# Optimization experiments

Measured on AMD Instinct MI355X. Metric: run time of the kernel, lower is better.

The kernel has to match this reference:

```python
import jax, jax.numpy as jnp
import numpy as np
import math

B, S, E = 4, 2048, 1024
H, KV = 16, 4            # query heads, kv heads
HD = E // H              # head_dim = 64
R, CD = 8, 64            # TPA rank, context dim
NQ, NL = 8, 2            # qubits, VQC layers
EPS = 1e-6
LN_EPS = 1e-5


def setup_inputs() -> dict:
    key = jax.random.key(0)
    ks = jax.random.split(key, 16)
    def dense(k, i, o):
        return (jax.random.normal(k, (i, o), jnp.float32) / np.float32(np.sqrt(i)))
    d = {}
    d["x"] = jax.random.normal(ks[0], (B, S, E), jnp.float32)
    d["ctxW"] = dense(ks[1], E, CD);      d["ctxb"] = jnp.zeros((CD,), jnp.float32)
    d["qaW"] = dense(ks[2], E, R * HD);   d["qab"] = jnp.zeros((R * HD,), jnp.float32)
    d["qbW"] = dense(ks[3], CD, R * H);   d["qbb"] = jnp.zeros((R * H,), jnp.float32)
    d["kaW"] = dense(ks[4], E, R * HD);   d["kab"] = jnp.zeros((R * HD,), jnp.float32)
    d["kbW"] = dense(ks[5], CD, R * KV);  d["kbb"] = jnp.zeros((R * KV,), jnp.float32)
    d["vaW"] = dense(ks[6], E, R * HD);   d["vab"] = jnp.zeros((R * HD,), jnp.float32)
    d["vbW"] = dense(ks[7], CD, R * KV);  d["vbb"] = jnp.zeros((R * KV,), jnp.float32)
    d["qeW"] = dense(ks[8], HD, NQ);      d["qeb"] = jnp.zeros((NQ,), jnp.float32)
    d["vqc"] = jax.random.normal(ks[9], (NL, NQ, 3), jnp.float32) * 0.3
    d["ent"] = jnp.array([0.1], jnp.float32)
    d["outW"] = dense(ks[10], E, E);      d["outb"] = jnp.zeros((E,), jnp.float32)
    d["gamma"] = jnp.ones((E,), jnp.float32)
    d["beta"] = jnp.zeros((E,), jnp.float32)
    return d


def _tpa(x, ctx, aW, ab, bW, bb, nh):
    # output = sum_r (x @ A_r) outer (ctx @ B_r)  ->  [b, nh, s, head_dim]
    b, s, _ = x.shape
    a = (x @ aW + ab).reshape(b, s, R, HD)
    bf = (ctx @ bW + bb).reshape(b, s, R, nh)
    return jnp.einsum('bsrd,bsrh->bhsd', a, bf)


def _quantum_features(x, qeW, qeb, vqc, ent):
    # x: [b, h, s, HD] -> features [b, h, s, 2*NQ]
    angles = jnp.tanh(x @ qeW + qeb) * math.pi
    f = angles
    for l in range(NL):
        p = vqc[l]  # [NQ, 3]
        f = jnp.cos(f + p[:, 0]) * jnp.sin(f + p[:, 1]) + jnp.cos(f + p[:, 2])
        f = f * (1.0 + ent[0] * jnp.roll(f, shift=1, axis=-1))  # entanglement
    qf = jnp.concatenate([jnp.cos(f), jnp.sin(f)], axis=-1)
    return qf / (jnp.linalg.norm(qf, axis=-1, keepdims=True) + EPS)


def reference(x, ctxW, ctxb, qaW, qab, qbW, qbb, kaW, kab, kbW, kbb,
              vaW, vab, vbW, vbb, qeW, qeb, vqc, ent, outW, outb, gamma, beta):
    ctx = x @ ctxW + ctxb                              # [B,S,CD]
    q = _tpa(x, ctx, qaW, qab, qbW, qbb, H)            # [B,H,S,HD]
    k = _tpa(x, ctx, kaW, kab, kbW, kbb, KV)           # [B,KV,S,HD]
    v = _tpa(x, ctx, vaW, vab, vbW, vbb, KV)
    # GQA: expand KV heads to match query heads
    k = jnp.repeat(k, H // KV, axis=1)
    v = jnp.repeat(v, H // KV, axis=1)
    qf = _quantum_features(q, qeW, qeb, vqc, ent)      # [B,H,S,2*NQ]
    kf = _quantum_features(k, qeW, qeb, vqc, ent)
    # causal linear attention via cumulative KV state
    kv = jnp.cumsum(jnp.einsum('bhsf,bhsd->bhsfd', kf, v), axis=2)
    num = jnp.einsum('bhsf,bhsfd->bhsd', qf, kv)
    den = jnp.einsum('bhsf,bhsf->bhs', qf, jnp.cumsum(kf, axis=2))
    attn = num / (den[..., None] + EPS)                # [B,H,S,HD]
    o = attn.transpose(0, 2, 1, 3).reshape(B, S, E) @ outW + outb
    y = x + o                                          # residual + layernorm
    mu = jnp.mean(y, axis=-1, keepdims=True)
    var = jnp.mean(jnp.square(y - mu), axis=-1, keepdims=True)
    return gamma * (y - mu) / jnp.sqrt(var + LN_EPS) + beta
```

## Files before the change

kernel.cpp:

```cpp
#include <hip/hip_runtime.h>
#include <math.h>

#define Bb  4
#define Ss  2048
#define Ee  1024
#define Hh  16
#define KVh 4
#define HD  64
#define RNK 8
#define CDd 64
#define NQ  8
#define NLn 2
#define NF  16
#define NC  32
#define CT  (Ss/NC)
#define BS  (Bb*Ss)
#define NCAT 1664

typedef unsigned short ushort_t;
typedef __attribute__((ext_vector_type(8))) short short8;
typedef __attribute__((ext_vector_type(4))) float f32x4;

__device__ __forceinline__ unsigned short f2bf(float f) {
    unsigned int u = __float_as_uint(f);
    unsigned int r = (u + 0x7FFFu + ((u >> 16) & 1u)) >> 16;
    return (unsigned short)r;
}
__device__ __forceinline__ float bf2f(unsigned short h) {
    return __uint_as_float(((unsigned int)h) << 16);
}

#define GLD16(gp, lp) \
    __builtin_amdgcn_global_load_lds((const __attribute__((address_space(1))) void*)(gp), \
                                     (__attribute__((address_space(3))) void*)(lp), 16, 0, 0)

__global__ __launch_bounds__(256)
void cast_f32_bf16(const float* __restrict__ in, ushort_t* __restrict__ outp, long n)
{
    long i = ((long)blockIdx.x * blockDim.x + threadIdx.x) * 8;
    if (i >= n) return;
    short8 o;
    #pragma unroll
    for (int j = 0; j < 8; ++j) o[j] = (short)f2bf(in[i + j]);
    *(short8*)(outp + i) = o;
}

__global__ __launch_bounds__(256)
void transpose_cast(const float* __restrict__ W, ushort_t* __restrict__ Wt,
                    int K, int Nsub, int nOff, int ldT)
{
    __shared__ float t[32][33];
    const int k0 = blockIdx.x * 32, n0 = blockIdx.y * 32;
    const int tx = threadIdx.x & 31, ty = threadIdx.x >> 5;
    #pragma unroll
    for (int i = 0; i < 4; ++i)
        t[ty + 8*i][tx] = W[(size_t)(k0 + ty + 8*i) * Nsub + (n0 + tx)];
    __syncthreads();
    #pragma unroll
    for (int i = 0; i < 4; ++i)
        Wt[(size_t)(nOff + n0 + ty + 8*i) * ldT + (k0 + tx)] = f2bf(t[tx][ty + 8*i]);
}

__global__ __launch_bounds__(256)
void transpose_cast3(const float* __restrict__ W0, const float* __restrict__ W1,
                     const float* __restrict__ W2, ushort_t* __restrict__ Wt, int ldT)
{
    __shared__ float t[32][33];
    const int z = blockIdx.z;
    const float* W = (z == 0) ? W0 : (z == 1) ? W1 : W2;
    const int nOff = 512 * z;
    const int k0 = blockIdx.x * 32, n0 = blockIdx.y * 32;
    const int tx = threadIdx.x & 31, ty = threadIdx.x >> 5;
    #pragma unroll
    for (int i = 0; i < 4; ++i)
        t[ty + 8*i][tx] = W[(size_t)(k0 + ty + 8*i) * 512 + (n0 + tx)];
    __syncthreads();
    #pragma unroll
    for (int i = 0; i < 4; ++i)
        Wt[(size_t)(nOff + n0 + ty + 8*i) * ldT + (k0 + tx)] = f2bf(t[tx][ty + 8*i]);
}

__global__ void build_bcat(const float* __restrict__ qab, const float* __restrict__ kab,
                           const float* __restrict__ vab, const float* __restrict__ ctxb,
                           float* __restrict__ bcat)
{
    int n = blockIdx.x * 256 + threadIdx.x;
    if (n >= NCAT) return;
    float v = 0.f;
    if      (n < 512)  v = qab[n];
    else if (n < 1024) v = kab[n - 512];
    else if (n < 1536) v = vab[n - 1024];
    else if (n < 1600) v = ctxb[n - 1536];
    bcat[n] = v;
}

template<int RES, int OUTBF>
__global__ __launch_bounds__(256)
void gemm_mfma(const ushort_t* __restrict__ A, const ushort_t* __restrict__ Bt,
               const float* __restrict__ bias, const float* __restrict__ res,
               void* __restrict__ Cout, int M, int N, int K)
{
    __shared__ ushort_t Al[128 * 32];
    __shared__ ushort_t Bl[128 * 32];
    const int tid  = threadIdx.x;
    const int lane = tid & 63;
    const int wave = tid >> 6;
    const int wm = wave >> 1;
    const int wn = wave & 1;

    const unsigned nx  = gridDim.x;
    const unsigned bid = blockIdx.y * nx + blockIdx.x;
    const unsigned nwg = nx * gridDim.y;
    const unsigned qc = nwg >> 3, rc = nwg & 7;
    const unsigned xc = bid & 7, of = bid >> 3;
    const unsigned tile = (xc < rc ? xc * (qc + 1) : rc * (qc + 1) + (xc - rc) * qc) + of;
    const int bm = (int)(tile / nx) * 128;
    const int bn = (int)(tile % nx) * 128;

    f32x4 acc[4][4] = {};

    const int arow0 = wave * 16 + (lane >> 2);
    const int kq = lane & 3;
    const ushort_t* Ag0 = A  + (size_t)(bm + arow0) * K + kq * 8;
    const ushort_t* Ag1 = A  + (size_t)(bm + 64 + arow0) * K + kq * 8;
    const ushort_t* Bg0 = Bt + (size_t)(bn + arow0) * K + kq * 8;
    const ushort_t* Bg1 = Bt + (size_t)(bn + 64 + arow0) * K + kq * 8;
    ushort_t* Alw = Al + wave * 512;
    ushort_t* Blw = Bl + wave * 512;

    const int fr = lane & 15;
    const int fg = lane >> 4;

    for (int k0 = 0; k0 < K; k0 += 32) {
        GLD16(Ag0 + k0, Alw);
        GLD16(Ag1 + k0, Alw + 2048);
        GLD16(Bg0 + k0, Blw);
        GLD16(Bg1 + k0, Blw + 2048);
        __syncthreads();
        short8 af[4], bfv[4];
        #pragma unroll
        for (int mi = 0; mi < 4; ++mi)
            af[mi] = *(const short8*)&Al[(wm*64 + mi*16 + fr) * 32 + fg * 8];
        #pragma unroll
        for (int ni = 0; ni < 4; ++ni)
            bfv[ni] = *(const short8*)&Bl[(wn*64 + ni*16 + fr) * 32 + fg * 8];
        #pragma unroll
        for (int mi = 0; mi < 4; ++mi)
            #pragma unroll
            for (int ni = 0; ni < 4; ++ni)
                acc[mi][ni] = __builtin_amdgcn_mfma_f32_16x16x32_bf16(
                    af[mi], bfv[ni], acc[mi][ni], 0, 0, 0);
        __syncthreads();
    }

    float bv[4];
    #pragma unroll
    for (int ni = 0; ni < 4; ++ni) bv[ni] = bias[bn + wn*64 + ni*16 + fr];
    #pragma unroll
    for (int mi = 0; mi < 4; ++mi) {
        #pragma unroll
        for (int ni = 0; ni < 4; ++ni) {
            const int gn = bn + wn*64 + ni*16 + fr;
            #pragma unroll
            for (int r = 0; r < 4; ++r) {
                const int gm = bm + wm*64 + mi*16 + fg*4 + r;
                float v = acc[mi][ni][r] + bv[ni];
                if (RES) v += res[(size_t)gm * N + gn];
                if (OUTBF) ((ushort_t*)Cout)[(size_t)gm * N + gn] = f2bf(v);
                else       ((float*)Cout)[(size_t)gm * N + gn] = v;
            }
        }
    }
}

__global__ __launch_bounds__(64)
void combine_quantum(const ushort_t* __restrict__ Cf,
                     const float* __restrict__ qbW, const float* __restrict__ qbb,
                     const float* __restrict__ kbW, const float* __restrict__ kbb,
                     const float* __restrict__ vbW, const float* __restrict__ vbb,
                     const float* __restrict__ qeW, const float* __restrict__ qeb,
                     const float* __restrict__ vqc, const float* __restrict__ ent,
                     float* __restrict__ qf_g, float* __restrict__ kf_g,
                     float* __restrict__ v_g)
{
    const int bs = blockIdx.x;
    const int b = bs >> 11;
    const int s = bs & 2047;
    const int d = threadIdx.x;

    __shared__ float ctx_l[CDd];
    __shared__ float bfq[128];
    __shared__ float bfk[32];
    __shared__ float bfv[32];
    __shared__ float qew_s[HD*NQ];
    __shared__ float rows[Hh+KVh][65];
    __shared__ float ang[Hh+KVh][NQ];

    const ushort_t* Crow = Cf + (size_t)bs * NCAT;
    ctx_l[d] = bf2f(Crow[1536 + d]);
    #pragma unroll
    for (int i = 0; i < 8; ++i)
        qew_s[d + 64*i] = qeW[d + 64*i];
    __syncthreads();

    {
        float q0 = qbb[d], q1 = qbb[d + 64];
        float kv = (d < 32) ? kbb[d] : vbb[d - 32];
        const float* Wkv = (d < 32) ? (kbW + d) : (vbW + (d - 32));
        #pragma unroll 8
        for (int k = 0; k < CDd; ++k) {
            const float c = ctx_l[k];
            q0 += c * qbW[(size_t)k*128 + d];
            q1 += c * qbW[(size_t)k*128 + d + 64];
            kv += c * Wkv[(size_t)k*32];
        }
        bfq[d] = q0; bfq[d + 64] = q1;
        if (d < 32) bfk[d] = kv; else bfv[d - 32] = kv;
    }

    float aq[RNK], ak[RNK], av[RNK];
    #pragma unroll
    for (int r = 0; r < RNK; ++r) {
        aq[r] = bf2f(Crow[r*64 + d]);
        ak[r] = bf2f(Crow[512 + r*64 + d]);
        av[r] = bf2f(Crow[1024 + r*64 + d]);
    }
    __syncthreads();

    #pragma unroll
    for (int h = 0; h < Hh; ++h) {
        float acc = 0.f;
        #pragma unroll
        for (int r = 0; r < RNK; ++r) acc += aq[r] * bfq[r*16 + h];
        rows[h][d] = acc;
    }
    #pragma unroll
    for (int kvh = 0; kvh < KVh; ++kvh) {
        float acck = 0.f, accv = 0.f;
        #pragma unroll
        for (int r = 0; r < RNK; ++r) {
            acck += ak[r] * bfk[r*4 + kvh];
            accv += av[r] * bfv[r*4 + kvh];
        }
        rows[Hh + kvh][d] = acck;
        v_g[((size_t)(b*KVh + kvh)*Ss + s)*HD + d] = accv;
    }
    __syncthreads();

    for (int task = d; task < (Hh+KVh)*NQ; task += 64) {
        const int row = task >> 3, i = task & 7;
        float acc = qeb[i];
        #pragma unroll 16
        for (int dd = 0; dd < HD; ++dd) acc += rows[row][dd] * qew_s[dd*8 + i];
        ang[row][i] = tanhf(acc) * 3.14159265358979323846f;
    }
    __syncthreads();

    if (d < Hh + KVh) {
        float f[NQ];
        #pragma unroll
        for (int i = 0; i < NQ; ++i) f[i] = ang[d][i];
        const float entv = ent[0];
        #pragma unroll
        for (int l = 0; l < NLn; ++l) {
            float g[NQ];
            #pragma unroll
            for (int i = 0; i < NQ; ++i) {
                const float p0 = vqc[(l*NQ + i)*3 + 0];
                const float p1 = vqc[(l*NQ + i)*3 + 1];
                const float p2 = vqc[(l*NQ + i)*3 + 2];
                g[i] = cosf(f[i] + p0) * sinf(f[i] + p1) + cosf(f[i] + p2);
            }
            #pragma unroll
            for (int i = 0; i < NQ; ++i)
                f[i] = g[i] * (1.f + entv * g[(i + 7) & 7]);
        }
        float c[NQ], sn[NQ], ss = 0.f;
        #pragma unroll
        for (int i = 0; i < NQ; ++i) {
            c[i] = cosf(f[i]); sn[i] = sinf(f[i]);
            ss += c[i]*c[i] + sn[i]*sn[i];
        }
        const float inv = 1.f / (sqrtf(ss) + 1e-6f);
        float* dst = (d < Hh)
            ? qf_g + ((size_t)(b*Hh + d)*Ss + s)*NF
            : kf_g + ((size_t)(b*KVh + (d - Hh))*Ss + s)*NF;
        #pragma unroll
        for (int i = 0; i < NQ; ++i) { dst[i] = c[i]*inv; dst[NQ+i] = sn[i]*inv; }
    }
}

__global__ __launch_bounds__(64)
void chunk_partial(const float* __restrict__ kf_g, const float* __restrict__ v_g,
                   float* __restrict__ kvpart, float* __restrict__ kfpart)
{
    const int id = blockIdx.x;
    const int c = id & (NC-1);
    const int bk = id / NC;
    const int d = threadIdx.x;
    __shared__ float kf_l[CT][NF];
    const int s0 = c * CT;
    const float* kfp = kf_g + ((size_t)bk*Ss + s0)*NF;
    #pragma unroll
    for (int t = 0; t < (CT*NF)/64; ++t)
        ((float*)kf_l)[d + 64*t] = kfp[d + 64*t];
    __syncthreads();
    float st[NF] = {};
    const float* vp = v_g + ((size_t)bk*Ss + s0)*HD;
    for (int t = 0; t < CT; ++t) {
        const float vd = vp[(size_t)t*HD + d];
        #pragma unroll
        for (int f = 0; f < NF; ++f) st[f] += kf_l[t][f] * vd;
    }
    float* kvp = kvpart + (size_t)id * (NF*HD);
    #pragma unroll
    for (int f = 0; f < NF; ++f) kvp[f*HD + d] = st[f];
    if (d < NF) {
        float acc = 0.f;
        for (int t = 0; t < CT; ++t) acc += kf_l[t][d];
        kfpart[(size_t)id*NF + d] = acc;
    }
}

__global__ void prefix_scan(float* __restrict__ kvpart, float* __restrict__ kfpart)
{
    const int idx = blockIdx.x * blockDim.x + threadIdx.x;
    const int total = Bb*KVh * (NF*HD + NF);
    if (idx >= total) return;
    const int bk = idx / (NF*HD + NF);
    const int e = idx % (NF*HD + NF);
    if (e < NF*HD) {
        float* p = kvpart + (size_t)bk*NC*(NF*HD) + e;
        float run = 0.f;
        for (int c = 0; c < NC; ++c) {
            const float t = p[(size_t)c*(NF*HD)];
            p[(size_t)c*(NF*HD)] = run;
            run += t;
        }
    } else {
        const int f = e - NF*HD;
        float* p = kfpart + (size_t)bk*NC*NF + f;
        float run = 0.f;
        for (int c = 0; c < NC; ++c) {
            const float t = p[(size_t)c*NF];
            p[(size_t)c*NF] = run;
            run += t;
        }
    }
}

__global__ __launch_bounds__(64)
void attn_scan(const float* __restrict__ qf_g, const float* __restrict__ kf_g,
               const float* __restrict__ v_g,
               const float* __restrict__ kvpart, const float* __restrict__ kfpart,
               ushort_t* __restrict__ o_bf)
{
    const int id = blockIdx.x;
    const int c = id & (NC-1);
    const int bh = id / NC;
    const int h = bh & (Hh-1);
    const int b = bh / Hh;
    const int kvh = h >> 2;
    const int d = threadIdx.x;
    __shared__ float kf_l[CT][NF];
    __shared__ float qf_l[CT][NF];
    const int s0 = c * CT;
    const float* kfp = kf_g + ((size_t)(b*KVh + kvh)*Ss + s0)*NF;
    const float* qfp = qf_g + ((size_t)(b*Hh + h)*Ss + s0)*NF;
    #pragma unroll
    for (int t = 0; t < (CT*NF)/64; ++t) {
        ((float*)kf_l)[d + 64*t] = kfp[d + 64*t];
        ((float*)qf_l)[d + 64*t] = qfp[d + 64*t];
    }
    float st[NF], kfs[NF];
    const float* kvp = kvpart + ((size_t)(b*KVh + kvh)*NC + c)*(NF*HD);
    const float* kfsp = kfpart + ((size_t)(b*KVh + kvh)*NC + c)*NF;
    #pragma unroll
    for (int f = 0; f < NF; ++f) { st[f] = kvp[f*HD + d]; kfs[f] = kfsp[f]; }
    __syncthreads();
    const float* vp = v_g + ((size_t)(b*KVh + kvh)*Ss + s0)*HD;
    ushort_t* op = o_bf + ((size_t)(b*Ss + s0))*Ee + h*HD;
    for (int t = 0; t < CT; ++t) {
        const float vd = vp[(size_t)t*HD + d];
        float num = 0.f, den = 0.f;
        #pragma unroll
        for (int f = 0; f < NF; ++f) {
            const float kv = kf_l[t][f];
            st[f]  += kv * vd;
            kfs[f] += kv;
            const float qv = qf_l[t][f];
            num += qv * st[f];
            den += qv * kfs[f];
        }
        op[(size_t)t*Ee + d] = f2bf(num / (den + 1e-6f));
    }
}

__global__ __launch_bounds__(256)
void layernorm_res(const float* __restrict__ x, const ushort_t* __restrict__ o_bf,
                   const float* __restrict__ gamma, const float* __restrict__ beta,
                   float* __restrict__ out)
{
    __shared__ float tmp[4];
    const int row = blockIdx.x;
    const int t = threadIdx.x;
    const float* xp = x + (size_t)row * Ee;
    const ushort_t* op = o_bf + (size_t)row * Ee;
    float v[4];
    float sum = 0.f;
    #pragma unroll
    for (int i = 0; i < 4; ++i) {
        const int n = t + 256*i;
        v[i] = xp[n] + bf2f(op[n]);
        sum += v[i];
    }
    #pragma unroll
    for (int o = 32; o > 0; o >>= 1) sum += __shfl_down(sum, o, 64);
    if ((t & 63) == 0) tmp[t >> 6] = sum;
    __syncthreads();
    const float mu = (tmp[0] + tmp[1] + tmp[2] + tmp[3]) * (1.f/Ee);
    __syncthreads();
    float vs = 0.f;
    #pragma unroll
    for (int i = 0; i < 4; ++i) { const float dd = v[i] - mu; vs += dd*dd; }
    #pragma unroll
    for (int o = 32; o > 0; o >>= 1) vs += __shfl_down(vs, o, 64);
    if ((t & 63) == 0) tmp[t >> 6] = vs;
    __syncthreads();
    const float var = (tmp[0] + tmp[1] + tmp[2] + tmp[3]) * (1.f/Ee);
    const float inv = rsqrtf(var + 1e-5f);
    float* pout = out + (size_t)row * Ee;
    #pragma unroll
    for (int i = 0; i < 4; ++i) {
        const int n = t + 256*i;
        pout[n] = gamma[n] * (v[i] - mu) * inv + beta[n];
    }
}

extern "C" void kernel_launch(void* const* d_in, const int* in_sizes, int n_in,
                              void* d_out, int out_size, void* d_ws, size_t ws_size,
                              hipStream_t stream)
{
    const float* x    = (const float*)d_in[0];
    const float* ctxW = (const float*)d_in[1];
    const float* ctxb = (const float*)d_in[2];
    const float* qaW  = (const float*)d_in[3];
    const float* qab  = (const float*)d_in[4];
    const float* qbW  = (const float*)d_in[5];
    const float* qbb  = (const float*)d_in[6];
    const float* kaW  = (const float*)d_in[7];
    const float* kab  = (const float*)d_in[8];
    const float* kbW  = (const float*)d_in[9];
    const float* kbb  = (const float*)d_in[10];
    const float* vaW  = (const float*)d_in[11];
    const float* vab  = (const float*)d_in[12];
    const float* vbW  = (const float*)d_in[13];
    const float* vbb  = (const float*)d_in[14];
    const float* qeW  = (const float*)d_in[15];
    const float* qeb  = (const float*)d_in[16];
    const float* vqc  = (const float*)d_in[17];
    const float* ent  = (const float*)d_in[18];
    const float* outW = (const float*)d_in[19];
    const float* outb = (const float*)d_in[20];
    const float* gamma= (const float*)d_in[21];
    const float* beta = (const float*)d_in[22];
    float* out = (float*)d_out;

    char* p = (char*)d_ws;
    auto alloc = [&](size_t bytes) { char* r = p; p += (bytes + 255) & ~(size_t)255; return (void*)r; };
    ushort_t* xb    = (ushort_t*)alloc((size_t)BS * Ee * 2);
    ushort_t* WcatT = (ushort_t*)alloc((size_t)NCAT * Ee * 2);
    ushort_t* outWt = (ushort_t*)alloc((size_t)Ee * Ee * 2);
    float*    bcat  = (float*)   alloc(NCAT * 4);
    ushort_t* Cf    = (ushort_t*)alloc((size_t)BS * NCAT * 2);
    float*    qf    = (float*)   alloc((size_t)Bb*Hh*Ss*NF * 4);
    float*    kf    = (float*)   alloc((size_t)Bb*KVh*Ss*NF * 4);
    float*    vg    = (float*)   alloc((size_t)Bb*KVh*Ss*HD * 4);
    float*    kvpart= (float*)   alloc((size_t)Bb*KVh*NC*NF*HD * 4);
    float*    kfpart= (float*)   alloc((size_t)Bb*KVh*NC*NF * 4);
    ushort_t* obf2  = (ushort_t*)alloc((size_t)BS * Ee * 2);
    ushort_t* obf   = Cf;

    cast_f32_bf16<<<(BS*(long)Ee/8 + 255)/256, 256, 0, stream>>>(x, xb, (long)BS*Ee);
    transpose_cast3<<<dim3(32, 16, 3), 256, 0, stream>>>(qaW, kaW, vaW, WcatT, Ee);
    transpose_cast<<<dim3(32, 2),  256, 0, stream>>>(ctxW, WcatT, Ee, 64,   1536, Ee);
    transpose_cast<<<dim3(32, 32), 256, 0, stream>>>(outW, outWt, Ee, 1024, 0,    Ee);
    hipMemsetAsync(WcatT + (size_t)1600 * Ee, 0, (size_t)64 * Ee * 2, stream);
    build_bcat<<<(NCAT + 255)/256, 256, 0, stream>>>(qab, kab, vab, ctxb, bcat);

    gemm_mfma<0,1><<<dim3(NCAT/128, BS/128), 256, 0, stream>>>(
        xb, WcatT, bcat, nullptr, Cf, BS, NCAT, Ee);
    combine_quantum<<<BS, 64, 0, stream>>>(Cf, qbW, qbb, kbW, kbb, vbW, vbb,
                                           qeW, qeb, vqc, ent, qf, kf, vg);
    chunk_partial<<<Bb*KVh*NC, 64, 0, stream>>>(kf, vg, kvpart, kfpart);
    prefix_scan<<<(Bb*KVh*(NF*HD + NF) + 255)/256, 256, 0, stream>>>(kvpart, kfpart);
    attn_scan<<<Bb*Hh*NC, 64, 0, stream>>>(qf, kf, vg, kvpart, kfpart, obf);
    gemm_mfma<0,1><<<dim3(Ee/128, BS/128), 256, 0, stream>>>(
        obf, outWt, outb, nullptr, obf2, BS, Ee, Ee);
    layernorm_res<<<BS, 256, 0, stream>>>(x, obf2, gamma, beta, out);
}
```

Baseline: 329.9 us.

## Parallelize quantum feature map across lanes, pack rows per block, merge prep kernels

The combine_quantum kernel now handles four sequence positions per 256-thread block. The VQC feature computation is spread across 8 lanes per head, using shuffles for the entanglement roll and the norm reduction, where before one thread did all 8 qubits serially with only 20 of 64 lanes active. The ctxW transpose, the memset and the bias build are merged into one prep kernel to cut launches. attn_scan splits its num/den accumulators into two chains to expose ILP. The risk is more shared memory per block and some redundant work on the inactive third stripe.

```diff
diff --git a/kernel.cpp b/kernel.cpp
--- a/kernel.cpp
+++ b/kernel.cpp
@@ -80,18 +80,39 @@
         Wt[(size_t)(nOff + n0 + ty + 8*i) * ldT + (k0 + tx)] = f2bf(t[tx][ty + 8*i]);
 }
 
-__global__ void build_bcat(const float* __restrict__ qab, const float* __restrict__ kab,
-                           const float* __restrict__ vab, const float* __restrict__ ctxb,
-                           float* __restrict__ bcat)
-{
-    int n = blockIdx.x * 256 + threadIdx.x;
-    if (n >= NCAT) return;
-    float v = 0.f;
-    if      (n < 512)  v = qab[n];
-    else if (n < 1024) v = kab[n - 512];
-    else if (n < 1536) v = vab[n - 1024];
-    else if (n < 1600) v = ctxb[n - 1536];
-    bcat[n] = v;
+__global__ __launch_bounds__(256)
+void prep_small(const float* __restrict__ ctxW,
+                const float* __restrict__ qab, const float* __restrict__ kab,
+                const float* __restrict__ vab, const float* __restrict__ ctxb,
+                ushort_t* __restrict__ WcatT, float* __restrict__ bcat)
+{
+    __shared__ float t[32][33];
+    const int bid = blockIdx.x;
+    if (bid < 64) {
+        const int k0 = (bid >> 1) * 32, n0 = (bid & 1) * 32;
+        const int tx = threadIdx.x & 31, ty = threadIdx.x >> 5;
+        #pragma unroll
+        for (int i = 0; i < 4; ++i)
+            t[ty + 8*i][tx] = ctxW[(size_t)(k0 + ty + 8*i) * 64 + (n0 + tx)];
+        __syncthreads();
+        #pragma unroll
+        for (int i = 0; i < 4; ++i)
+            WcatT[(size_t)(1536 + n0 + ty + 8*i) * Ee + (k0 + tx)] = f2bf(t[tx][ty + 8*i]);
+    } else if (bid < 96) {
+        const int idx = (bid - 64) * 2048 + threadIdx.x * 8;
+        short8 z = {0, 0, 0, 0, 0, 0, 0, 0};
+        *(short8*)(WcatT + (size_t)1600 * Ee + idx) = z;
+    } else {
+        const int n = (bid - 96) * 256 + threadIdx.x;
+        if (n < NCAT) {
+            float v = 0.f;
+            if      (n < 512)  v = qab[n];
+            else if (n < 1024) v = kab[n - 512];
+            else if (n < 1536) v = vab[n - 1024];
+            else if (n < 1600) v = ctxb[n - 1536];
+            bcat[n] = v;
+        }
+    }
 }
 
 template<int RES, int OUTBF>
@@ -173,7 +194,7 @@
     }
 }
 
-__global__ __launch_bounds__(64)
+__global__ __launch_bounds__(256)
 void combine_quantum(const ushort_t* __restrict__ Cf,
                      const float* __restrict__ qbW, const float* __restrict__ qbb,
                      const float* __restrict__ kbW, const float* __restrict__ kbb,
@@ -183,24 +204,25 @@
                      float* __restrict__ qf_g, float* __restrict__ kf_g,
                      float* __restrict__ v_g)
 {
-    const int bs = blockIdx.x;
+    const int wid = threadIdx.x >> 6;
+    const int d   = threadIdx.x & 63;
+    const int bs  = blockIdx.x * 4 + wid;
     const int b = bs >> 11;
     const int s = bs & 2047;
-    const int d = threadIdx.x;
-
-    __shared__ float ctx_l[CDd];
-    __shared__ float bfq[128];
-    __shared__ float bfk[32];
-    __shared__ float bfv[32];
+
     __shared__ float qew_s[HD*NQ];
-    __shared__ float rows[Hh+KVh][65];
-    __shared__ float ang[Hh+KVh][NQ];
+    __shared__ float ctx_l[4][CDd];
+    __shared__ float bfq[4][128];
+    __shared__ float bfk[4][32];
+    __shared__ float bfv[4][32];
+    __shared__ float rows[4][Hh+KVh][65];
+
+    #pragma unroll
+    for (int i = 0; i < 2; ++i)
+        qew_s[threadIdx.x + 256*i] = qeW[threadIdx.x + 256*i];
 
     const ushort_t* Crow = Cf + (size_t)bs * NCAT;
-    ctx_l[d] = bf2f(Crow[1536 + d]);
-    #pragma unroll
-    for (int i = 0; i < 8; ++i)
-        qew_s[d + 64*i] = qeW[d + 64*i];
+    ctx_l[wid][d] = bf2f(Crow[1536 + d]);
     __syncthreads();
 
     {
@@ -209,13 +231,13 @@
         const float* Wkv = (d < 32) ? (kbW + d) : (vbW + (d - 32));
         #pragma unroll 8
         for (int k = 0; k < CDd; ++k) {
-            const float c = ctx_l[k];
+            const float c = ctx_l[wid][k];
             q0 += c * qbW[(size_t)k*128 + d];
             q1 += c * qbW[(size_t)k*128 + d + 64];
             kv += c * Wkv[(size_t)k*32];
         }
-        bfq[d] = q0; bfq[d + 64] = q1;
-        if (d < 32) bfk[d] = kv; else bfv[d - 32] = kv;
+        bfq[wid][d] = q0; bfq[wid][d + 64] = q1;
+        if (d < 32) bfk[wid][d] = kv; else bfv[wid][d - 32] = kv;
     }
 
     float aq[RNK], ak[RNK], av[RNK];
@@ -231,62 +253,58 @@
     for (int h = 0; h < Hh; ++h) {
         float acc = 0.f;
         #pragma unroll
-        for (int r = 0; r < RNK; ++r) acc += aq[r] * bfq[r*16 + h];
-        rows[h][d] = acc;
+        for (int r = 0; r < RNK; ++r) acc += aq[r] * bfq[wid][r*16 + h];
+        rows[wid][h][d] = acc;
     }
     #pragma unroll
     for (int kvh = 0; kvh < KVh; ++kvh) {
         float acck = 0.f, accv = 0.f;
         #pragma unroll
         for (int r = 0; r < RNK; ++r) {
-            acck += ak[r] * bfk[r*4 + kvh];
-            accv += av[r] * bfv[r*4 + kvh];
-        }
-        rows[Hh + kvh][d] = acck;
+            acck += ak[r] * bfk[wid][r*4 + kvh];
+            accv += av[r] * bfv[wid][r*4 + kvh];
+        }
+        rows[wid][Hh + kvh][d] = acck;
         v_g[((size_t)(b*KVh + kvh)*Ss + s)*HD + d] = accv;
     }
     __syncthreads();
 
-    for (int task = d; task < (Hh+KVh)*NQ; task += 64) {
-        const int row = task >> 3, i = task & 7;
-        float acc = qeb[i];
+    const float entv = ent[0];
+    const int i   = d & 7;
+    const int src = (d & ~7) | ((i + 7) & 7);
+    float p00 = vqc[(0*NQ + i)*3 + 0], p01 = vqc[(0*NQ + i)*3 + 1], p02 = vqc[(0*NQ + i)*3 + 2];
+    float p10 = vqc[(1*NQ + i)*3 + 0], p11 = vqc[(1*NQ + i)*3 + 1], p12 = vqc[(1*NQ + i)*3 + 2];
+    const float qebi = qeb[i];
+
+    #pragma unroll
+    for (int stripe = 0; stripe < 3; ++stripe) {
+        const int row = stripe * 8 + (d >> 3);
+        const bool active = (row < Hh + KVh);
+        const int rowc = active ? row : (Hh + KVh - 1);
+        float acc = qebi;
         #pragma unroll 16
-        for (int dd = 0; dd < HD; ++dd) acc += rows[row][dd] * qew_s[dd*8 + i];
-        ang[row][i] = tanhf(acc) * 3.14159265358979323846f;
-    }
-    __syncthreads();
-
-    if (d < Hh + KVh) {
-        float f[NQ];
-        #pragma unroll
-        for (int i = 0; i < NQ; ++i) f[i] = ang[d][i];
-        const float entv = ent[0];
-        #pragma unroll
-        for (int l = 0; l < NLn; ++l) {
-            float g[NQ];
-            #pragma unroll
-            for (int i = 0; i < NQ; ++i) {
-                const float p0 = vqc[(l*NQ + i)*3 + 0];
-                const float p1 = vqc[(l*NQ + i)*3 + 1];
-                const float p2 = vqc[(l*NQ + i)*3 + 2];
-                g[i] = cosf(f[i] + p0) * sinf(f[i] + p1) + cosf(f[i] + p2);
-            }
-            #pragma unroll
-            for (int i = 0; i < NQ; ++i)
-                f[i] = g[i] * (1.f + entv * g[(i + 7) & 7]);
-        }
-        float c[NQ], sn[NQ], ss = 0.f;
-        #pragma unroll
-        for (int i = 0; i < NQ; ++i) {
-            c[i] = cosf(f[i]); sn[i] = sinf(f[i]);
-            ss += c[i]*c[i] + sn[i]*sn[i];
-        }
+        for (int dd = 0; dd < HD; ++dd)
+            acc += rows[wid][rowc][dd] * qew_s[dd*8 + i];
+        float f = tanhf(acc) * 3.14159265358979323846f;
+        float g = cosf(f + p00) * sinf(f + p01) + cosf(f + p02);
+        float gp = __shfl(g, src, 64);
+        f = g * (1.f + entv * gp);
+        g = cosf(f + p10) * sinf(f + p11) + cosf(f + p12);
+        gp = __shfl(g, src, 64);
+        f = g * (1.f + entv * gp);
+        float c = cosf(f), sn = sinf(f);
+        float ss = c*c + sn*sn;
+        ss += __shfl_xor(ss, 1, 64);
+        ss += __shfl_xor(ss, 2, 64);
+        ss += __shfl_xor(ss, 4, 64);
         const float inv = 1.f / (sqrtf(ss) + 1e-6f);
-        float* dst = (d < Hh)
-            ? qf_g + ((size_t)(b*Hh + d)*Ss + s)*NF
-            : kf_g + ((size_t)(b*KVh + (d - Hh))*Ss + s)*NF;
-        #pragma unroll
-        for (int i = 0; i < NQ; ++i) { dst[i] = c[i]*inv; dst[NQ+i] = sn[i]*inv; }
+        if (active) {
+            float* dst = (row < Hh)
+                ? qf_g + ((size_t)(b*Hh + row)*Ss + s)*NF
+                : kf_g + ((size_t)(b*KVh + (row - Hh))*Ss + s)*NF;
+            dst[i]      = c * inv;
+            dst[NQ + i] = sn * inv;
+        }
     }
 }
 
@@ -382,17 +400,19 @@
     ushort_t* op = o_bf + ((size_t)(b*Ss + s0))*Ee + h*HD;
     for (int t = 0; t < CT; ++t) {
         const float vd = vp[(size_t)t*HD + d];
-        float num = 0.f, den = 0.f;
-        #pragma unroll
-        for (int f = 0; f < NF; ++f) {
-            const float kv = kf_l[t][f];
-            st[f]  += kv * vd;
-            kfs[f] += kv;
-            const float qv = qf_l[t][f];
-            num += qv * st[f];
-            den += qv * kfs[f];
-        }
-        op[(size_t)t*Ee + d] = f2bf(num / (den + 1e-6f));
+        float num0 = 0.f, num1 = 0.f, den0 = 0.f, den1 = 0.f;
+        #pragma unroll
+        for (int f = 0; f < NF; f += 2) {
+            const float kv0 = kf_l[t][f];
+            const float kv1 = kf_l[t][f+1];
+            st[f]   += kv0 * vd;   kfs[f]   += kv0;
+            st[f+1] += kv1 * vd;   kfs[f+1] += kv1;
+            const float qv0 = qf_l[t][f];
+            const float qv1 = qf_l[t][f+1];
+            num0 += qv0 * st[f];   den0 += qv0 * kfs[f];
+            num1 += qv1 * st[f+1]; den1 += qv1 * kfs[f+1];
+        }
+        op[(size_t)t*Ee + d] = f2bf((num0 + num1) / ((den0 + den1) + 1e-6f));
     }
 }
 
@@ -483,15 +503,13 @@
 
     cast_f32_bf16<<<(BS*(long)Ee/8 + 255)/256, 256, 0, stream>>>(x, xb, (long)BS*Ee);
     transpose_cast3<<<dim3(32, 16, 3), 256, 0, stream>>>(qaW, kaW, vaW, WcatT, Ee);
-    transpose_cast<<<dim3(32, 2),  256, 0, stream>>>(ctxW, WcatT, Ee, 64,   1536, Ee);
-    transpose_cast<<<dim3(32, 32), 256, 0, stream>>>(outW, outWt, Ee, 1024, 0,    Ee);
-    hipMemsetAsync(WcatT + (size_t)1600 * Ee, 0, (size_t)64 * Ee * 2, stream);
-    build_bcat<<<(NCAT + 255)/256, 256, 0, stream>>>(qab, kab, vab, ctxb, bcat);
+    prep_small<<<103, 256, 0, stream>>>(ctxW, qab, kab, vab, ctxb, WcatT, bcat);
+    transpose_cast<<<dim3(32, 32), 256, 0, stream>>>(outW, outWt, Ee, 1024, 0, Ee);
 
     gemm_mfma<0,1><<<dim3(NCAT/128, BS/128), 256, 0, stream>>>(
         xb, WcatT, bcat, nullptr, Cf, BS, NCAT, Ee);
-    combine_quantum<<<BS, 64, 0, stream>>>(Cf, qbW, qbb, kbW, kbb, vbW, vbb,
-                                           qeW, qeb, vqc, ent, qf, kf, vg);
+    combine_quantum<<<BS/4, 256, 0, stream>>>(Cf, qbW, qbb, kbW, kbb, vbW, vbb,
+                                              qeW, qeb, vqc, ent, qf, kf, vg);
     chunk_partial<<<Bb*KVh*NC, 64, 0, stream>>>(kf, vg, kvpart, kfpart);
     prefix_scan<<<(Bb*KVh*(NF*HD + NF) + 255)/256, 256, 0, stream>>>(kvpart, kfpart);
     attn_scan<<<Bb*Hh*NC, 64, 0, stream>>>(qf, kf, vg, kvpart, kfpart, obf);
```

Result: faster. 301.9 us (-8.5%).
